# Performance work log

Measured on AMD Instinct MI355X. Metric: run time of the kernel, lower is better.

Reference implementation:

```python
import jax, jax.numpy as jnp
import numpy as np


def _sample_choices(prob_weights, key):
    # softmax over edge-type dim, take P(NORMAL_EDGE)=index 1
    prob_edge = jax.nn.softmax(prob_weights, axis=-1)[..., 1]  # [out, in]
    k_bern, k_fix = jax.random.split(key)
    choices = jax.random.bernoulli(k_bern, prob_edge).astype(prob_weights.dtype)  # [out, in]
    # zero-connection fixup: rows with no sampled edge get one random connection
    out_f, in_f = choices.shape
    conn_count = jnp.sum(choices, axis=-1)  # [out]
    rand_cols = jax.random.randint(k_fix, (out_f,), 0, in_f)  # [out]
    fix = ((conn_count == 0)[:, None] & (jnp.arange(in_f)[None, :] == rand_cols[:, None]))
    choices = choices + fix.astype(choices.dtype)
    # selected edges -> 0, unselected -> 1 (min operator branch; no *-1 negation)
    mask = jnp.abs(choices - 1.0)
    return mask


def reference(x, prob_weights):
    # x: [B, in], prob_weights: [out, in, 2]
    mask = _sample_choices(prob_weights, jax.random.key(42))  # [out, in]
    # result[b, o] = min_i (x[b, i] + mask[o, i])  -- [B, out, in] intermediate
    operator_inputs = x[:, None, :] + mask[None, :, :]
    return jnp.min(operator_inputs, axis=-1)  # [B, out]


def setup_inputs() -> dict:
    key = jax.random.key(0)
    k_x, k_w = jax.random.split(key)
    B, IN, OUT = 512, 512, 512
    x = jax.random.uniform(k_x, (B, IN), dtype=jnp.float32)
    prob_weights = jax.random.uniform(k_w, (OUT, IN, 2), dtype=jnp.float32)
    return {"x": x, "prob_weights": prob_weights}
```

## Files before the change

### kernel.cpp

```cpp
#include <hip/hip_runtime.h>
#include <cstdint>

__host__ __device__ inline void threefry2x32(uint32_t k0, uint32_t k1,
                                             uint32_t x0, uint32_t x1,
                                             uint32_t& o0, uint32_t& o1) {
  const uint32_t ks2 = k0 ^ k1 ^ 0x1BD11BDAu;
  uint32_t v0 = x0 + k0, v1 = x1 + k1;
#define RL(v, r) (((v) << (r)) | ((v) >> (32 - (r))))
#define RND4(a, b, c, d)                                                       \
  v0 += v1; v1 = RL(v1, a); v1 ^= v0;                                          \
  v0 += v1; v1 = RL(v1, b); v1 ^= v0;                                          \
  v0 += v1; v1 = RL(v1, c); v1 ^= v0;                                          \
  v0 += v1; v1 = RL(v1, d); v1 ^= v0;
  RND4(13, 15, 26, 6)  v0 += k1;  v1 += ks2 + 1u;
  RND4(17, 29, 16, 24) v0 += ks2; v1 += k0 + 2u;
  RND4(13, 15, 26, 6)  v0 += k0;  v1 += k1 + 3u;
  RND4(17, 29, 16, 24) v0 += k1;  v1 += ks2 + 4u;
  RND4(13, 15, 26, 6)  v0 += ks2; v1 += k0 + 5u;
#undef RND4
#undef RL
  o0 = v0; o1 = v1;
}

#define IN_F 512
#define OUT_F 512
#define BATCH 512

__global__ __launch_bounds__(512) void gen_mask_kernel(
    const float* __restrict__ pw, float* __restrict__ M,
    uint32_t kb0, uint32_t kb1, uint32_t kl0, uint32_t kl1) {
  const int o = blockIdx.x;
  const int i = threadIdx.x;

  const float2 w = ((const float2*)pw)[o * IN_F + i];
  const float mx = fmaxf(w.x, w.y);
  const float e0 = expf(w.x - mx);
  const float e1 = expf(w.y - mx);
  const float p = e1 / (e0 + e1);

  const uint32_t n = (uint32_t)(o * IN_F + i);
  uint32_t h0, h1;
  threefry2x32(kb0, kb1, 0u, n, h0, h1);
  const uint32_t bits = h0 ^ h1;
  const float u = __uint_as_float((bits >> 9) | 0x3F800000u) - 1.0f;
  const bool c = u < p;

  __shared__ unsigned long long words[8];
  __shared__ int cnt;
  if (i == 0) cnt = 0;
  __syncthreads();
  const unsigned long long bal = __ballot(c);
  if ((i & 63) == 0) {
    words[i >> 6] = bal;
    atomicAdd(&cnt, __popcll(bal));
  }
  __syncthreads();
  if (cnt == 0 && i == 0) {
    uint32_t c0, c1;
    threefry2x32(kl0, kl1, 0u, (uint32_t)o, c0, c1);
    const uint32_t rb = c0 ^ c1;
    const uint32_t col = rb & (IN_F - 1);
    words[col >> 6] |= (1ull << (col & 63u));
  }
  __syncthreads();
  const bool sel = (words[i >> 6] >> (i & 63)) & 1ull;
  M[o * IN_F + i] = sel ? 0.0f : 1e9f;
}

#define BT 64
#define OT 64
#define KT 32
#define NZ 4
#define KZ (IN_F / NZ)

__global__ __launch_bounds__(256) void minplus_kernel(
    const float* __restrict__ x, const float* __restrict__ M,
    float* __restrict__ part) {
  __shared__ float xs[KT][BT + 4];
  __shared__ float ms[KT][OT + 4];

  const int tid = threadIdx.x;
  const int tx = tid & 15;
  const int ty = tid >> 4;
  const int b0 = blockIdx.x * BT;
  const int o0 = blockIdx.y * OT;
  const int kb = blockIdx.z * KZ;

  const int lr = tid >> 3;
  const int lc = (tid & 7) * 4;

  float4 acc[4];
#pragma unroll
  for (int i = 0; i < 4; ++i) acc[i] = make_float4(1e30f, 1e30f, 1e30f, 1e30f);

  for (int kt = 0; kt < KZ; kt += KT) {
#pragma unroll
    for (int j = 0; j < 2; ++j) {
      const int r = j * 32 + lr;
      const float4 v = *(const float4*)&x[(b0 + r) * IN_F + kb + kt + lc];
      xs[lc + 0][r] = v.x; xs[lc + 1][r] = v.y;
      xs[lc + 2][r] = v.z; xs[lc + 3][r] = v.w;
      const float4 w = *(const float4*)&M[(o0 + r) * IN_F + kb + kt + lc];
      ms[lc + 0][r] = w.x; ms[lc + 1][r] = w.y;
      ms[lc + 2][r] = w.z; ms[lc + 3][r] = w.w;
    }
    __syncthreads();
#pragma unroll 8
    for (int k = 0; k < KT; ++k) {
      const float4 xv = *(const float4*)&xs[k][tx * 4];
      const float4 mv = *(const float4*)&ms[k][ty * 4];
#pragma unroll
      for (int i = 0; i < 4; ++i) {
        const float xi = (i == 0) ? xv.x : (i == 1) ? xv.y : (i == 2) ? xv.z : xv.w;
        acc[i].x = fminf(acc[i].x, xi + mv.x);
        acc[i].y = fminf(acc[i].y, xi + mv.y);
        acc[i].z = fminf(acc[i].z, xi + mv.z);
        acc[i].w = fminf(acc[i].w, xi + mv.w);
      }
    }
    __syncthreads();
  }

  float* pz = part + (size_t)blockIdx.z * (BATCH * OUT_F);
#pragma unroll
  for (int i = 0; i < 4; ++i)
    *(float4*)&pz[(size_t)(b0 + 4 * tx + i) * OUT_F + o0 + 4 * ty] = acc[i];
}

__global__ __launch_bounds__(256) void reduce_kernel(
    const float* __restrict__ part, float* __restrict__ out) {
  const int n = blockIdx.x * 256 + threadIdx.x;
  float4 a = ((const float4*)part)[n];
#pragma unroll
  for (int z = 1; z < NZ; ++z) {
    const float4 b = ((const float4*)(part + (size_t)z * BATCH * OUT_F))[n];
    a.x = fminf(a.x, b.x); a.y = fminf(a.y, b.y);
    a.z = fminf(a.z, b.z); a.w = fminf(a.w, b.w);
  }
  ((float4*)out)[n] = a;
}

extern "C" void kernel_launch(void* const* d_in, const int* in_sizes, int n_in,
                              void* d_out, int out_size, void* d_ws, size_t ws_size,
                              hipStream_t stream) {
  (void)in_sizes; (void)n_in; (void)out_size; (void)ws_size;
  const float* x = (const float*)d_in[0];
  const float* pw = (const float*)d_in[1];
  float* M = (float*)d_ws;
  float* part = (float*)d_ws + BATCH * OUT_F;
  float* out = (float*)d_out;

  uint32_t kb0, kb1, kf0, kf1, kl0, kl1;
  threefry2x32(0u, 42u, 0u, 0u, kb0, kb1);
  threefry2x32(0u, 42u, 0u, 1u, kf0, kf1);
  threefry2x32(kf0, kf1, 0u, 1u, kl0, kl1);

  gen_mask_kernel<<<dim3(OUT_F), dim3(IN_F), 0, stream>>>(pw, M, kb0, kb1, kl0, kl1);
  minplus_kernel<<<dim3(BATCH / BT, OUT_F / OT, NZ), dim3(256), 0, stream>>>(x, M, part);
  reduce_kernel<<<dim3(BATCH * OUT_F / 4 / 256), dim3(256), 0, stream>>>(part, out);
}
```

Before: 77.26 us.

## Fuse mask generation, min-plus and reduction into one cooperative kernel

Merges the three kernels (mask generation, split-K min-plus, partial reduction) into a single cooperative launch of 256 blocks separated by grid-wide syncs. Each block generates two mask rows, then does its min-plus tile, then reduces a slice of the partials. This removes two kernel launch boundaries and their tail gaps, at the cost of grid-sync overhead and a cooperative-launch requirement that all blocks be co-resident.

```diff
diff --git a/kernel.cpp b/kernel.cpp
--- a/kernel.cpp
+++ b/kernel.cpp
@@ -1,5 +1,8 @@
 #include <hip/hip_runtime.h>
+#include <hip/hip_cooperative_groups.h>
 #include <cstdint>
+
+namespace cg = cooperative_groups;
 
 __host__ __device__ inline void threefry2x32(uint32_t k0, uint32_t k1,
                                              uint32_t x0, uint32_t x1,
@@ -26,60 +29,73 @@
 #define OUT_F 512
 #define BATCH 512
 
-__global__ __launch_bounds__(512) void gen_mask_kernel(
-    const float* __restrict__ pw, float* __restrict__ M,
-    uint32_t kb0, uint32_t kb1, uint32_t kl0, uint32_t kl1) {
-  const int o = blockIdx.x;
-  const int i = threadIdx.x;
-
-  const float2 w = ((const float2*)pw)[o * IN_F + i];
-  const float mx = fmaxf(w.x, w.y);
-  const float e0 = expf(w.x - mx);
-  const float e1 = expf(w.y - mx);
-  const float p = e1 / (e0 + e1);
-
-  const uint32_t n = (uint32_t)(o * IN_F + i);
-  uint32_t h0, h1;
-  threefry2x32(kb0, kb1, 0u, n, h0, h1);
-  const uint32_t bits = h0 ^ h1;
-  const float u = __uint_as_float((bits >> 9) | 0x3F800000u) - 1.0f;
-  const bool c = u < p;
-
-  __shared__ unsigned long long words[8];
-  __shared__ int cnt;
-  if (i == 0) cnt = 0;
-  __syncthreads();
-  const unsigned long long bal = __ballot(c);
-  if ((i & 63) == 0) {
-    words[i >> 6] = bal;
-    atomicAdd(&cnt, __popcll(bal));
-  }
-  __syncthreads();
-  if (cnt == 0 && i == 0) {
-    uint32_t c0, c1;
-    threefry2x32(kl0, kl1, 0u, (uint32_t)o, c0, c1);
-    const uint32_t rb = c0 ^ c1;
-    const uint32_t col = rb & (IN_F - 1);
-    words[col >> 6] |= (1ull << (col & 63u));
-  }
-  __syncthreads();
-  const bool sel = (words[i >> 6] >> (i & 63)) & 1ull;
-  M[o * IN_F + i] = sel ? 0.0f : 1e9f;
-}
-
 #define BT 64
 #define OT 64
 #define KT 32
 #define NZ 4
 #define KZ (IN_F / NZ)
 
-__global__ __launch_bounds__(256) void minplus_kernel(
-    const float* __restrict__ x, const float* __restrict__ M,
-    float* __restrict__ part) {
+__global__ __launch_bounds__(256) void fused_kernel(
+    const float* __restrict__ x, const float* __restrict__ pw,
+    float* __restrict__ M, float* __restrict__ part, float* __restrict__ out,
+    uint32_t kb0, uint32_t kb1, uint32_t kl0, uint32_t kl1) {
+  const int tid = threadIdx.x;
+  const int bid = (blockIdx.z * 8 + blockIdx.y) * 8 + blockIdx.x;
+
+  __shared__ unsigned long long words[8];
+  __shared__ int cnt;
+#pragma unroll 1
+  for (int r = 0; r < 2; ++r) {
+    const int o = bid * 2 + r;
+    if (tid == 0) cnt = 0;
+    __syncthreads();
+    bool cj[2];
+#pragma unroll
+    for (int j = 0; j < 2; ++j) {
+      const int i = tid + 256 * j;
+      const float2 w = ((const float2*)pw)[o * IN_F + i];
+      const float mx = fmaxf(w.x, w.y);
+      const float e0 = expf(w.x - mx);
+      const float e1 = expf(w.y - mx);
+      const float p = e1 / (e0 + e1);
+      const uint32_t n = (uint32_t)(o * IN_F + i);
+      uint32_t h0, h1;
+      threefry2x32(kb0, kb1, 0u, n, h0, h1);
+      const uint32_t bits = h0 ^ h1;
+      const float u = __uint_as_float((bits >> 9) | 0x3F800000u) - 1.0f;
+      cj[j] = u < p;
+    }
+#pragma unroll
+    for (int j = 0; j < 2; ++j) {
+      const unsigned long long bal = __ballot(cj[j]);
+      if ((tid & 63) == 0) {
+        words[(tid >> 6) + 4 * j] = bal;
+        atomicAdd(&cnt, __popcll(bal));
+      }
+    }
+    __syncthreads();
+    if (cnt == 0 && tid == 0) {
+      uint32_t c0, c1;
+      threefry2x32(kl0, kl1, 0u, (uint32_t)o, c0, c1);
+      const uint32_t col = (c0 ^ c1) & (IN_F - 1);
+      words[col >> 6] |= (1ull << (col & 63u));
+    }
+    __syncthreads();
+#pragma unroll
+    for (int j = 0; j < 2; ++j) {
+      const int i = tid + 256 * j;
+      const bool sel = (words[i >> 6] >> (i & 63)) & 1ull;
+      M[o * IN_F + i] = sel ? 0.0f : 1e9f;
+    }
+    __syncthreads();
+  }
+
+  __threadfence();
+  cg::this_grid().sync();
+
   __shared__ float xs[KT][BT + 4];
   __shared__ float ms[KT][OT + 4];
 
-  const int tid = threadIdx.x;
   const int tx = tid & 15;
   const int ty = tid >> 4;
   const int b0 = blockIdx.x * BT;
@@ -96,13 +112,13 @@
   for (int kt = 0; kt < KZ; kt += KT) {
 #pragma unroll
     for (int j = 0; j < 2; ++j) {
-      const int r = j * 32 + lr;
-      const float4 v = *(const float4*)&x[(b0 + r) * IN_F + kb + kt + lc];
-      xs[lc + 0][r] = v.x; xs[lc + 1][r] = v.y;
-      xs[lc + 2][r] = v.z; xs[lc + 3][r] = v.w;
-      const float4 w = *(const float4*)&M[(o0 + r) * IN_F + kb + kt + lc];
-      ms[lc + 0][r] = w.x; ms[lc + 1][r] = w.y;
-      ms[lc + 2][r] = w.z; ms[lc + 3][r] = w.w;
+      const int rr = j * 32 + lr;
+      const float4 v = *(const float4*)&x[(b0 + rr) * IN_F + kb + kt + lc];
+      xs[lc + 0][rr] = v.x; xs[lc + 1][rr] = v.y;
+      xs[lc + 2][rr] = v.z; xs[lc + 3][rr] = v.w;
+      const float4 w = *(const float4*)&M[(o0 + rr) * IN_F + kb + kt + lc];
+      ms[lc + 0][rr] = w.x; ms[lc + 1][rr] = w.y;
+      ms[lc + 2][rr] = w.z; ms[lc + 3][rr] = w.w;
     }
     __syncthreads();
 #pragma unroll 8
@@ -125,19 +141,19 @@
 #pragma unroll
   for (int i = 0; i < 4; ++i)
     *(float4*)&pz[(size_t)(b0 + 4 * tx + i) * OUT_F + o0 + 4 * ty] = acc[i];
-}
 
-__global__ __launch_bounds__(256) void reduce_kernel(
-    const float* __restrict__ part, float* __restrict__ out) {
-  const int n = blockIdx.x * 256 + threadIdx.x;
-  float4 a = ((const float4*)part)[n];
+  __threadfence();
+  cg::this_grid().sync();
+
+  const int g = bid * 256 + tid;
+  float4 a = ((const float4*)part)[g];
 #pragma unroll
   for (int z = 1; z < NZ; ++z) {
-    const float4 b = ((const float4*)(part + (size_t)z * BATCH * OUT_F))[n];
+    const float4 b = ((const float4*)(part + (size_t)z * BATCH * OUT_F))[g];
     a.x = fminf(a.x, b.x); a.y = fminf(a.y, b.y);
     a.z = fminf(a.z, b.z); a.w = fminf(a.w, b.w);
   }
-  ((float4*)out)[n] = a;
+  ((float4*)out)[g] = a;
 }
 
 extern "C" void kernel_launch(void* const* d_in, const int* in_sizes, int n_in,
@@ -155,7 +171,9 @@
   threefry2x32(0u, 42u, 0u, 1u, kf0, kf1);
   threefry2x32(kf0, kf1, 0u, 1u, kl0, kl1);
 
-  gen_mask_kernel<<<dim3(OUT_F), dim3(IN_F), 0, stream>>>(pw, M, kb0, kb1, kl0, kl1);
-  minplus_kernel<<<dim3(BATCH / BT, OUT_F / OT, NZ), dim3(256), 0, stream>>>(x, M, part);
-  reduce_kernel<<<dim3(BATCH * OUT_F / 4 / 256), dim3(256), 0, stream>>>(part, out);
+  void* args[] = {(void*)&x, (void*)&pw, (void*)&M, (void*)&part, (void*)&out,
+                  (void*)&kb0, (void*)&kb1, (void*)&kl0, (void*)&kl1};
+  hipLaunchCooperativeKernel((const void*)fused_kernel,
+                             dim3(BATCH / BT, OUT_F / OT, NZ), dim3(256),
+                             args, 0, stream);
 }
```

After: 180.7 us. 134% more time.
